# Optimization experiments

Measured on AMD Instinct MI355X. Metric: run time of the kernel, lower is better.

## Reference

```python
import jax, jax.numpy as jnp
import numpy as np

C = 256      # embed_dim
GROUP = 2    # conv groups
K = 3        # kernel/pool size
K2 = K * K
OG = 8       # offset groups (hard-coded in Similarity_cal)
NEX = 3      # exemplars per image (out_conv expects group*3*4 channels)


def conv2d(x, w, b, pad):
    y = jax.lax.conv_general_dilated(x, w, (1, 1), [(pad, pad), (pad, pad)],
                                     dimension_numbers=("NCHW", "OIHW", "NCHW"))
    return y + b[None, :, None, None]


def ln_c(x, g, b, eps=1e-5):
    # LayerNorm over the channel axis of NCHW (torch permutes to NHWC, LN, permute back)
    mu = x.mean(axis=1, keepdims=True)
    var = ((x - mu) ** 2).mean(axis=1, keepdims=True)
    return (x - mu) / jnp.sqrt(var + eps) * g[None, :, None, None] + b[None, :, None, None]


def bilinear_gather(img, py, px):
    # img [Cg,H,W]; py,px [K2,H,W] -> samples [Cg,K2,H,W], zero outside borders
    Cg, H, W = img.shape
    y0f = jnp.floor(py); x0f = jnp.floor(px)
    wy = py - y0f; wx = px - x0f
    y0 = y0f.astype(jnp.int32); x0 = x0f.astype(jnp.int32)
    flat = img.reshape(Cg, H * W)

    def corner(yy, xx, w):
        valid = (yy >= 0) & (yy < H) & (xx >= 0) & (xx < W)
        idx = jnp.clip(yy, 0, H - 1) * W + jnp.clip(xx, 0, W - 1)
        v = jnp.take(flat, idx.reshape(-1), axis=1).reshape(Cg, K2, H, W)
        return v * (w * valid)[None]

    return (corner(y0, x0, (1 - wy) * (1 - wx)) + corner(y0, x0 + 1, (1 - wy) * wx)
            + corner(y0 + 1, x0, wy * (1 - wx)) + corner(y0 + 1, x0 + 1, wy * wx))


def deform_conv(x, offset, mask, weight, dilation):
    # x [C,H,W]; offset [2*OG*K2,H,W]; mask [OG*K2,H,W] (softmaxed); weight [NEX*GROUP, C//GROUP, K, K]
    Cc, H, W = x.shape
    pad = (K - 1) * dilation // 2
    off = offset.reshape(OG, K2, 2, H, W)  # (dy, dx) per offset-group / tap
    kk = jnp.arange(K, dtype=x.dtype)
    ky = jnp.repeat(kk, K) * dilation - pad  # [K2]
    kx = jnp.tile(kk, K) * dilation - pad
    ii = jnp.arange(H, dtype=x.dtype)
    jj = jnp.arange(W, dtype=x.dtype)
    py = ii[None, None, :, None] + ky[None, :, None, None] + off[:, :, 0]  # [OG,K2,H,W]
    px = jj[None, None, None, :] + kx[None, :, None, None] + off[:, :, 1]
    xg = x.reshape(OG, Cc // OG, H, W)
    samp = jax.vmap(bilinear_gather)(xg, py, px)              # [OG,Cg,K2,H,W]
    samp = samp * mask.reshape(OG, 1, K2, H, W)               # modulation
    samp = samp.reshape(GROUP, Cc // GROUP, K2, H, W)
    wR = weight.reshape(NEX * GROUP, Cc // GROUP, K2)
    gidx = jnp.arange(NEX * GROUP) // NEX                     # out-channel -> conv group
    return jnp.einsum("rck,rckhw->rhw", wR, samp[gidx])       # [NEX*GROUP,H,W]


def forward(querys_feat, supports_feat, in_w, in_b, ln_g, ln_b, out_w, out_b,
            offw1, offb1, mskw1, mskb1, offw2, offb2, mskw2, mskb2,
            offw4, offb4, mskw4, mskb4):
    B = querys_feat.shape[0]
    q = ln_c(conv2d(querys_feat, in_w, in_b, 0), ln_g, ln_b)                 # [B,C,H,W]
    s = supports_feat.reshape(B * NEX, C, K, K)
    s = ln_c(conv2d(s, in_w, in_b, 0), ln_g, ln_b).reshape(B, NEX, C, K, K)

    def offs(wo, bo, wm, bm):
        o = conv2d(q, wo, bo, (K - 1) // 2)
        m = jax.nn.softmax(conv2d(q, wm, bm, (K - 1) // 2), axis=1)  # softmax over all OG*K2 channels
        return o, m

    o1, m1 = offs(offw1, offb1, mskw1, mskb1)
    o2, m2 = offs(offw2, offb2, mskw2, mskb2)
    o4, m4 = offs(offw4, offb4, mskw4, mskb4)

    def per_sample(qi, si, o1i, m1i, o2i, m2i, o4i, m4i):
        w = si.reshape(NEX * GROUP, C // GROUP, K, K)         # dynamic per-exemplar kernels
        pooled = si.max(axis=(2, 3)).reshape(NEX * GROUP, C // GROUP)
        gidx = jnp.arange(NEX * GROUP) // NEX
        qg = qi.reshape(GROUP, C // GROUP, *qi.shape[1:])
        sim0 = jnp.einsum("rc,rchw->rhw", pooled, qg[gidx])   # grouped 1x1 conv branch
        d1 = deform_conv(qi, o1i, m1i, w, 1)
        d2 = deform_conv(qi, o2i, m2i, w, 2)
        d4 = deform_conv(qi, o4i, m4i, w, 4)
        return jnp.concatenate([sim0, d1, d2, d4], axis=0)    # [GROUP*3*4, H, W]

    sim = jax.vmap(per_sample)(q, s, o1, m1, o2, m2, o4, m4)
    return conv2d(sim, out_w, out_b, 0)                        # [B,C,H,W]


def setup_inputs() -> dict:
    key = jax.random.key(0)
    ks = jax.random.split(key, 20)
    B, H, W = 2, 96, 96
    inp = {
        "querys_feat": jax.random.normal(ks[0], (B, C, H, W), jnp.float32),
        "supports_feat": jax.random.normal(ks[1], (B, NEX, C, K, K), jnp.float32),
        "in_w": jax.random.normal(ks[2], (C, C, 1, 1), jnp.float32) / 16.0,
        "in_b": jax.random.normal(ks[3], (C,), jnp.float32) * 0.02,
        "ln_g": jnp.ones((C,), jnp.float32),
        "ln_b": jnp.zeros((C,), jnp.float32),
        "out_w": jax.random.normal(ks[4], (C, GROUP * 3 * 4, 1, 1), jnp.float32) * 0.2,
        "out_b": jax.random.normal(ks[5], (C,), jnp.float32) * 0.02,
    }
    i = 6
    for d in (1, 2, 4):
        inp[f"offw{d}"] = jax.random.normal(ks[i], (2 * OG * K2, C, K, K), jnp.float32) * 0.01; i += 1
        inp[f"offb{d}"] = jax.random.normal(ks[i], (2 * OG * K2,), jnp.float32) * 0.1; i += 1
        inp[f"mskw{d}"] = jax.random.normal(ks[i], (OG * K2, C, K, K), jnp.float32) * 0.02; i += 1
        inp[f"mskb{d}"] = jax.random.normal(ks[i], (OG * K2,), jnp.float32) * 0.1; i += 1
    return inp


def reference(querys_feat, supports_feat, in_w, in_b, ln_g, ln_b, out_w, out_b,
              offw1, offb1, mskw1, mskb1, offw2, offb2, mskw2, mskb2,
              offw4, offb4, mskw4, mskb4):
    return forward(querys_feat, supports_feat, in_w, in_b, ln_g, ln_b, out_w, out_b,
                   offw1, offb1, mskw1, mskb1, offw2, offb2, mskw2, mskb2,
                   offw4, offb4, mskw4, mskb4)
```

## Files before the change

### kernel.cpp

```cpp
#include <hip/hip_runtime.h>
#include <hip/hip_bf16.h>
#include <math.h>

#define HH 96
#define WWID 96
#define HW 9216
#define CC 256
#define BB 2
#define PROW 104
#define PCOL 128
#define PPX (PROW * PCOL)

typedef float f32x4 __attribute__((ext_vector_type(4)));
typedef _Float16 f16x8 __attribute__((ext_vector_type(8)));
typedef _Float16 h2v __attribute__((ext_vector_type(2)));

__device__ inline unsigned int pack2h(float a, float b) {
  unsigned short ua = __builtin_bit_cast(unsigned short, (_Float16)a);
  unsigned short ub = __builtin_bit_cast(unsigned short, (_Float16)b);
  return (unsigned int)ua | ((unsigned int)ub << 16);
}
__device__ inline float h_lo(unsigned int u) {
  return (float)__builtin_bit_cast(_Float16, (unsigned short)(u & 0xffffu));
}
__device__ inline float h_hi(unsigned int u) {
  return (float)__builtin_bit_cast(_Float16, (unsigned short)(u >> 16));
}

#if defined(__has_builtin)
#if __has_builtin(__builtin_amdgcn_fdot2)
#define FDOT2(a, b, c) __builtin_amdgcn_fdot2((a), (b), (c), false)
#endif
#endif
#ifndef FDOT2
#define FDOT2(a, b, c) ((c) + (float)(a).x * (float)(b).x + (float)(a).y * (float)(b).y)
#endif

__device__ inline void gload_lds16(const void* g, void* l) {
  __builtin_amdgcn_global_load_lds(
      (const __attribute__((address_space(1))) void*)g,
      (__attribute__((address_space(3))) void*)l, 16, 0, 0);
}

__global__ void k_transpose_w(const float* __restrict__ in_w, float* __restrict__ wT) {
  int k = blockIdx.x, c = threadIdx.x;
  wT[k * CC + c] = in_w[c * CC + k];
}

__global__ void k_packw(const float* __restrict__ ow1, const float* __restrict__ ob1,
                        const float* __restrict__ mw1, const float* __restrict__ mb1,
                        const float* __restrict__ ow2, const float* __restrict__ ob2,
                        const float* __restrict__ mw2, const float* __restrict__ mb2,
                        const float* __restrict__ ow4, const float* __restrict__ ob4,
                        const float* __restrict__ mw4, const float* __restrict__ mb4,
                        _Float16* __restrict__ Whf, float* __restrict__ Ball) {
  int idx = blockIdx.x * 256 + threadIdx.x;
  if (idx >= 3 * 256 * 2304) return;
  int d = idx / (256 * 2304);
  int rem = idx - d * 256 * 2304;
  int co = rem / 2304;
  int k = rem - co * 2304;
  int j = k >> 8, ci = k & 255;
  const float* ow = d == 0 ? ow1 : (d == 1 ? ow2 : ow4);
  const float* mw = d == 0 ? mw1 : (d == 1 ? mw2 : mw4);
  float v = 0.f;
  if (co < 144) v = ow[co * 2304 + ci * 9 + j];
  else if (co < 216) v = mw[(co - 144) * 2304 + ci * 9 + j];
  Whf[idx] = (_Float16)v;
  if (idx < 768) {
    int dd = idx >> 8, cc = idx & 255;
    const float* obv = dd == 0 ? ob1 : (dd == 1 ? ob2 : ob4);
    const float* mbv = dd == 0 ? mb1 : (dd == 1 ? mb2 : mb4);
    float bv = 0.f;
    if (cc < 144) bv = obv[cc];
    else if (cc < 216) bv = mbv[cc - 144];
    Ball[idx] = bv;
  }
}

__global__ void k_conv1_ln_q(const float* __restrict__ qin, const float* __restrict__ wT,
                             const float* __restrict__ in_b, const float* __restrict__ ln_g,
                             const float* __restrict__ ln_b, float* __restrict__ q_hwc,
                             _Float16* __restrict__ qpad) {
  int bx = blockIdx.x;
  int b = bx / 288;
  int hw0 = (bx % 288) * 32;
  int t = threadIdx.x;
  int lane = t & 63;
  int wv_id = t >> 6;
  __shared__ float xs[32 * 260];
  const float* qb = qin + (size_t)b * CC * HW;
  #pragma unroll
  for (int i = 0; i < 32; ++i) {
    int idx = t + i * 256;
    int p = idx & 31;
    int k = idx >> 5;
    xs[p * 260 + k] = qb[k * HW + hw0 + p];
  }
  __syncthreads();
  float acc[8][4];
  #pragma unroll
  for (int p = 0; p < 8; ++p) { acc[p][0]=0.f; acc[p][1]=0.f; acc[p][2]=0.f; acc[p][3]=0.f; }
  const float4* wT4 = (const float4*)wT;
  int p0 = wv_id * 8;
  for (int k = 0; k < 256; k += 4) {
    float4 w0 = wT4[(k + 0) * 64 + lane];
    float4 w1 = wT4[(k + 1) * 64 + lane];
    float4 w2 = wT4[(k + 2) * 64 + lane];
    float4 w3 = wT4[(k + 3) * 64 + lane];
    #pragma unroll
    for (int p = 0; p < 8; ++p) {
      float4 xv = *(const float4*)&xs[(p0 + p) * 260 + k];
      acc[p][0] += w0.x * xv.x + w1.x * xv.y + w2.x * xv.z + w3.x * xv.w;
      acc[p][1] += w0.y * xv.x + w1.y * xv.y + w2.y * xv.z + w3.y * xv.w;
      acc[p][2] += w0.z * xv.x + w1.z * xv.y + w2.z * xv.z + w3.z * xv.w;
      acc[p][3] += w0.w * xv.x + w1.w * xv.y + w2.w * xv.z + w3.w * xv.w;
    }
  }
  float4 bb = ((const float4*)in_b)[lane];
  float4 g4 = ((const float4*)ln_g)[lane];
  float4 b4 = ((const float4*)ln_b)[lane];
  #pragma unroll
  for (int p = 0; p < 8; ++p) {
    float y0 = acc[p][0] + bb.x, y1 = acc[p][1] + bb.y;
    float y2 = acc[p][2] + bb.z, y3 = acc[p][3] + bb.w;
    float s1 = y0 + y1 + y2 + y3;
    float s2 = y0*y0 + y1*y1 + y2*y2 + y3*y3;
    #pragma unroll
    for (int off = 32; off; off >>= 1) { s1 += __shfl_xor(s1, off); s2 += __shfl_xor(s2, off); }
    float mu = s1 * (1.f / 256.f);
    float rstd = rsqrtf(s2 * (1.f / 256.f) - mu * mu + 1e-5f);
    float4 o;
    o.x = (y0 - mu) * rstd * g4.x + b4.x;
    o.y = (y1 - mu) * rstd * g4.y + b4.y;
    o.z = (y2 - mu) * rstd * g4.z + b4.z;
    o.w = (y3 - mu) * rstd * g4.w + b4.w;
    int hw = hw0 + p0 + p;
    ((float4*)q_hwc)[((size_t)b * HW + hw) * 64 + lane] = o;
    int hh = hw / 96, ww = hw - hh * 96;
    int ppx = (hh + 4) * PCOL + ww + 4;
    struct alignas(8) h4 { _Float16 h[4]; };
    h4 oh;
    oh.h[0] = (_Float16)o.x; oh.h[1] = (_Float16)o.y;
    oh.h[2] = (_Float16)o.z; oh.h[3] = (_Float16)o.w;
    *(h4*)(qpad + ((size_t)b * PPX + ppx) * CC + lane * 4) = oh;
  }
}

__global__ void k_conv1_ln_s(const float* __restrict__ sup, const float* __restrict__ wT,
                             const float* __restrict__ in_b, const float* __restrict__ ln_g,
                             const float* __restrict__ ln_b, float* __restrict__ s_ln,
                             float* __restrict__ pooled) {
  int img = blockIdx.x;
  int t = threadIdx.x;
  __shared__ float xs[2304];
  __shared__ float red1[256], red2[256];
  #pragma unroll
  for (int p = 0; p < 9; ++p) xs[t * 9 + p] = sup[(size_t)img * 2304 + t * 9 + p];
  __syncthreads();
  float acc[9];
  #pragma unroll
  for (int p = 0; p < 9; ++p) acc[p] = 0.f;
  for (int k = 0; k < 256; ++k) {
    float wv = wT[k * CC + t];
    #pragma unroll
    for (int p = 0; p < 9; ++p) acc[p] += wv * xs[k * 9 + p];
  }
  float bias = in_b[t];
  #pragma unroll
  for (int p = 0; p < 9; ++p) acc[p] += bias;
  float g = ln_g[t], be = ln_b[t];
  float vals[9];
  #pragma unroll
  for (int p = 0; p < 9; ++p) {
    red1[t] = acc[p]; red2[t] = acc[p] * acc[p];
    __syncthreads();
    for (int s = 128; s > 0; s >>= 1) {
      if (t < s) { red1[t] += red1[t + s]; red2[t] += red2[t + s]; }
      __syncthreads();
    }
    float mu = red1[0] * (1.f / 256.f);
    float var = red2[0] * (1.f / 256.f) - mu * mu;
    float rstd = rsqrtf(var + 1e-5f);
    vals[p] = (acc[p] - mu) * rstd * g + be;
    __syncthreads();
  }
  #pragma unroll
  for (int p = 0; p < 9; ++p) s_ln[(size_t)img * 2304 + t * 9 + p] = vals[p];
  float mx = vals[0];
  #pragma unroll
  for (int p = 1; p < 9; ++p) mx = fmaxf(mx, vals[p]);
  int b = img / 3, e = img % 3;
  pooled[((size_t)b * 6 + e * 2 + (t >> 7)) * 128 + (t & 127)] = mx;
}


#define BAR() __builtin_amdgcn_s_barrier()
#define SCHEDB() __builtin_amdgcn_sched_barrier(0)
#define VMCNT(N) asm volatile("s_waitcnt vmcnt(" #N ")" ::: "memory")

#define MMA_ONE(M, N, S, QM, QN) \
  acc[(QM)*4+(M)][(QN)*2+(N)] = __builtin_amdgcn_mfma_f32_16x16x32_f16( \
      af[M][S], bf[(QN)*2+(N)][S], acc[(QM)*4+(M)][(QN)*2+(N)], 0, 0, 0);

#define MMA_Q(QM, QN) { \
  __builtin_amdgcn_s_setprio(1); \
  MMA_ONE(0,0,0,QM,QN) MMA_ONE(1,0,0,QM,QN) MMA_ONE(2,0,0,QM,QN) MMA_ONE(3,0,0,QM,QN) \
  MMA_ONE(0,1,0,QM,QN) MMA_ONE(1,1,0,QM,QN) MMA_ONE(2,1,0,QM,QN) MMA_ONE(3,1,0,QM,QN) \
  MMA_ONE(0,0,1,QM,QN) MMA_ONE(1,0,1,QM,QN) MMA_ONE(2,0,1,QM,QN) MMA_ONE(3,0,1,QM,QN) \
  MMA_ONE(0,1,1,QM,QN) MMA_ONE(1,1,1,QM,QN) MMA_ONE(2,1,1,QM,QN) MMA_ONE(3,1,1,QM,QN) \
  __builtin_amdgcn_s_setprio(0); }

#define LDA(BUF, QM) { \
  const char* p_ = smemB + (BUF) * 65536 + (wm * 128 + (QM) * 64 + l15) * 128; \
  af[0][0] = *(const f16x8*)(p_ + 0*2048 + rc0); af[0][1] = *(const f16x8*)(p_ + 0*2048 + rc1); \
  af[1][0] = *(const f16x8*)(p_ + 1*2048 + rc0); af[1][1] = *(const f16x8*)(p_ + 1*2048 + rc1); \
  af[2][0] = *(const f16x8*)(p_ + 2*2048 + rc0); af[2][1] = *(const f16x8*)(p_ + 2*2048 + rc1); \
  af[3][0] = *(const f16x8*)(p_ + 3*2048 + rc0); af[3][1] = *(const f16x8*)(p_ + 3*2048 + rc1); }

#define LDB(BUF, QN) { \
  const char* p_ = smemB + (BUF) * 65536 + 32768 + (wn * 64 + (QN) * 32 + l15) * 128; \
  bf[(QN)*2+0][0] = *(const f16x8*)(p_ + 0*2048 + rc0); bf[(QN)*2+0][1] = *(const f16x8*)(p_ + 0*2048 + rc1); \
  bf[(QN)*2+1][0] = *(const f16x8*)(p_ + 1*2048 + rc0); bf[(QN)*2+1][1] = *(const f16x8*)(p_ + 1*2048 + rc1); }

#define STAGEA(TILE, Q) { \
  gload_lds16(aBase + (size_t)((Q) * 64) * 2304 + (TILE) * 64, \
              smemB + ((TILE) & 1) * 65536 + (((Q) * 64 + wv * 8) * 128)); \
  gload_lds16(aBase + (size_t)(128 + (Q) * 64) * 2304 + (TILE) * 64, \
              smemB + ((TILE) & 1) * 65536 + ((128 + (Q) * 64 + wv * 8) * 128)); }

#define STAGEB(TILE, Q, PPX0, PPX1) { \
  int j_ = (TILE) >> 2; \
  int offp_ = (j_ / 3 - 1) * PCOL + (j_ % 3) - 1; \
  int cb_ = ((TILE) & 3) * 64; \
  int rs_ = (wv >> 2) * 64 + (Q) * 32 + (wv & 3) * 8; \
  gload_lds16(bBase + (size_t)((PPX0) + offp_) * CC + cb_, \
              smemB + ((TILE) & 1) * 65536 + 32768 + (rs_ * 128)); \
  gload_lds16(bBase + (size_t)((PPX1) + offp_) * CC + cb_, \
              smemB + ((TILE) & 1) * 65536 + 32768 + ((128 + rs_) * 128)); }

__global__ void __launch_bounds__(512) k_conv3_mfma8(
    const _Float16* __restrict__ qpad, const _Float16* __restrict__ Whf,
    float* __restrict__ offbuf, float* __restrict__ mskbuf) {
  int nb = blockIdx.x;
  int z = blockIdx.y;
  int d = z >> 1, b = z & 1;
  int t = threadIdx.x;
  int lane = t & 63, wv = t >> 6;
  int wm = wv >> 2, wn = wv & 3;
  int quad = lane >> 4, l15 = lane & 15;
  int l8 = lane >> 3, c7 = lane & 7;

  __shared__ _Float16 __attribute__((aligned(16))) smem[65536];
  char* smemB = (char*)smem;

  const _Float16* Wd = Whf + (size_t)d * 256 * 2304;
  const _Float16* qb = qpad + (size_t)b * PPX * CC;

  int scol = ((c7 ^ l8) << 3);
  int rc0 = ((quad ^ (l15 & 7)) << 4);
  int rc1 = (((4 | quad) ^ (l15 & 7)) << 4);

  const _Float16* aBase = Wd + (size_t)(wv * 8 + l8) * 2304 + scol;
  const _Float16* bBase = qb + scol;

  int ppx00, ppx01, ppx10, ppx11;
  {
    int rbase = (wv >> 2) * 64 + (wv & 3) * 8 + l8;
    int px, hh, ww;
    px = nb * 256 + rbase;             hh = px / 96; ww = px - hh * 96; ppx00 = (hh + 4) * PCOL + ww + 4;
    px = nb * 256 + 128 + rbase;       hh = px / 96; ww = px - hh * 96; ppx01 = (hh + 4) * PCOL + ww + 4;
    px = nb * 256 + 32 + rbase;        hh = px / 96; ww = px - hh * 96; ppx10 = (hh + 4) * PCOL + ww + 4;
    px = nb * 256 + 160 + rbase;       hh = px / 96; ww = px - hh * 96; ppx11 = (hh + 4) * PCOL + ww + 4;
  }

  f32x4 acc[8][4];
  #pragma unroll
  for (int i = 0; i < 8; ++i)
    #pragma unroll
    for (int j = 0; j < 4; ++j) acc[i][j] = (f32x4){0.f, 0.f, 0.f, 0.f};

  f16x8 af[4][2], bf[4][2];

  STAGEA(0, 0);
  STAGEB(0, 1, ppx10, ppx11);
  STAGEA(0, 1);
  STAGEB(0, 0, ppx00, ppx01);
  STAGEA(1, 0);
  STAGEB(1, 1, ppx10, ppx11);
  VMCNT(4);
  BAR();
  SCHEDB();

  #pragma unroll 1
  for (int ii = 0; ii < 17; ++ii) {
    int ta = 2 * ii + 1, tb = 2 * ii + 2, tc = 2 * ii + 3;
    LDA(0, 0) LDB(0, 0)
    STAGEA(ta, 1);
    BAR(); MMA_Q(0, 0); BAR();
    LDB(0, 1)
    STAGEB(ta, 0, ppx00, ppx01);
    BAR(); MMA_Q(0, 1); BAR();
    LDA(0, 1)
    STAGEA(tb, 0);
    BAR(); MMA_Q(1, 1); BAR();
    STAGEB(tb, 1, ppx10, ppx11);
    VMCNT(4);
    BAR(); SCHEDB(); MMA_Q(1, 0); BAR();
    LDA(1, 0) LDB(1, 0)
    STAGEA(tb, 1);
    BAR(); MMA_Q(0, 0); BAR();
    LDB(1, 1)
    STAGEB(tb, 0, ppx00, ppx01);
    BAR(); MMA_Q(0, 1); BAR();
    LDA(1, 1)
    STAGEA(tc, 0);
    BAR(); MMA_Q(1, 1); BAR();
    STAGEB(tc, 1, ppx10, ppx11);
    VMCNT(4);
    BAR(); SCHEDB(); MMA_Q(1, 0); BAR();
  }

  LDA(0, 0) LDB(0, 0)
  STAGEA(35, 1);
  BAR(); MMA_Q(0, 0); BAR();
  LDB(0, 1)
  STAGEB(35, 0, ppx00, ppx01);
  BAR(); MMA_Q(0, 1); BAR();
  LDA(0, 1)
  BAR(); MMA_Q(1, 1); BAR();
  VMCNT(0);
  BAR(); SCHEDB(); MMA_Q(1, 0); BAR();
  LDA(1, 0) LDB(1, 0)
  BAR(); MMA_Q(0, 0); BAR();
  LDB(1, 1)
  BAR(); MMA_Q(0, 1); BAR();
  LDA(1, 1)
  BAR(); MMA_Q(1, 1); BAR();
  MMA_Q(1, 0);

  float* obP = offbuf + (size_t)(d * BB + b) * 144 * HW;
  float* mkP = mskbuf + (size_t)(d * BB + b) * 72 * HW;
  #pragma unroll
  for (int mi = 0; mi < 8; ++mi) {
    int co = wm * 128 + mi * 16 + quad * 4;
    #pragma unroll
    for (int ni = 0; ni < 4; ++ni) {
      int px = nb * 256 + wn * 64 + ni * 16 + l15;
      f32x4 v = acc[mi][ni];
      #pragma unroll
      for (int r = 0; r < 4; ++r) {
        int c2 = co + r;
        if (c2 < 144) obP[(size_t)c2 * HW + px] = v[r];
        else if (c2 < 216) mkP[(size_t)(c2 - 144) * HW + px] = v[r];
      }
    }
  }
}

__global__ void k_taps(const float* __restrict__ offbuf, const float* __restrict__ mskbuf,
                       const float* __restrict__ Ball, unsigned int* __restrict__ taprec) {
  int t = threadIdx.x;
  int sub = t & 7, pxl = t >> 3;
  int bx = blockIdx.x;
  int z = bx / 288;
  int px = (bx - z * 288) * 32 + pxl;
  int d = z >> 1;
  const float* Bd = Ball + d * 256;
  const float* mp = mskbuf + (size_t)z * 72 * HW + px;
  float lg[9];
  float mx = -1e30f;
  #pragma unroll
  for (int j = 0; j < 9; ++j) {
    int tk = sub + 8 * j;
    lg[j] = mp[(size_t)tk * HW] + Bd[144 + tk];
    mx = fmaxf(mx, lg[j]);
  }
  mx = fmaxf(mx, __shfl_xor(mx, 1));
  mx = fmaxf(mx, __shfl_xor(mx, 2));
  mx = fmaxf(mx, __shfl_xor(mx, 4));
  float s = 0.f;
  #pragma unroll
  for (int j = 0; j < 9; ++j) s += __expf(lg[j] - mx);
  s += __shfl_xor(s, 1);
  s += __shfl_xor(s, 2);
  s += __shfl_xor(s, 4);
  float rinv = 1.f / s;
  int dil = 1 << (z >> 1);
  int h = px / WWID, w = px - h * WWID;
  const float* ob = offbuf + (size_t)z * 144 * HW + px;
  int k = sub;
  #pragma unroll
  for (int j = 0; j < 9; ++j) {
    int tk = sub + 8 * j;
    float dy = ob[(size_t)(tk * 2 + 0) * HW] + Bd[tk * 2 + 0];
    float dx = ob[(size_t)(tk * 2 + 1) * HW] + Bd[tk * 2 + 1];
    float m = __expf(lg[j] - mx) * rinv;
    float py = (float)(h + (k / 3) * dil - dil) + dy;
    float pxx = (float)(w + (k % 3) * dil - dil) + dx;
    float y0f = floorf(py), x0f = floorf(pxx);
    int y0 = (int)y0f, x0 = (int)x0f;
    float wy = py - y0f, wx = pxx - x0f;
    bool vy0 = (unsigned)y0 < 96u, vy1 = (unsigned)(y0 + 1) < 96u;
    bool vx0 = (unsigned)x0 < 96u, vx1 = (unsigned)(x0 + 1) < 96u;
    float w00 = (vy0 && vx0) ? (1.f - wy) * (1.f - wx) * m : 0.f;
    float w01 = (vy0 && vx1) ? (1.f - wy) * wx * m : 0.f;
    float w10 = (vy1 && vx0) ? wy * (1.f - wx) * m : 0.f;
    float w11 = (vy1 && vx1) ? wy * wx * m : 0.f;
    int iy = min(max(y0 + 4, 0), 102);
    int ix = min(max(x0 + 4, 0), 126);
    unsigned int* r = taprec + (((size_t)(z * 72 + tk)) * HW + px) * 3;
    r[0] = pack2h(w00, w01);
    r[1] = pack2h(w10, w11);
    r[2] = (unsigned int)(iy * PCOL + ix);
    k += 8; if (k >= 9) k -= 9;
  }
}

__global__ void k_sim0(const float* __restrict__ qt, const float* __restrict__ pooled,
                       float* __restrict__ sim) {
  int b = blockIdx.z, h = blockIdx.y, seg = blockIdx.x;
  int t = threadIdx.x;
  int pxl = t >> 5, lane = t & 31;
  int wcol = seg * 8 + pxl;
  int hw = h * WWID + wcol;
  __shared__ float plds[768];
  for (int i = t; i < 768; i += 256) plds[i] = pooled[(size_t)b * 768 + i];
  __syncthreads();
  const float* qtb = qt + (size_t)b * HW * CC;
  float acc[6] = {0.f, 0.f, 0.f, 0.f, 0.f, 0.f};
  #pragma unroll
  for (int m = 0; m < 8; ++m) {
    int cfull = m * 32 + lane;
    float qv = qtb[(size_t)hw * CC + cfull];
    if (m < 4) {
      int cp = cfull;
      acc[0] += plds[0 * 128 + cp] * qv;
      acc[1] += plds[1 * 128 + cp] * qv;
      acc[2] += plds[2 * 128 + cp] * qv;
    } else {
      int cp = cfull - 128;
      acc[3] += plds[3 * 128 + cp] * qv;
      acc[4] += plds[4 * 128 + cp] * qv;
      acc[5] += plds[5 * 128 + cp] * qv;
    }
  }
  #pragma unroll
  for (int r = 0; r < 6; ++r) {
    float v = acc[r];
    #pragma unroll
    for (int off = 16; off; off >>= 1) v += __shfl_down(v, off, 32);
    if (lane == 0) sim[((size_t)b * 24 + r) * HW + hw] = v;
  }
}

#define DO_P(U0, U1, IDX, P) { \
  h2v u0_ = __builtin_bit_cast(h2v, (U0)); \
  h2v u1_ = __builtin_bit_cast(h2v, (U1)); \
  const h2v* b0_ = qc + (size_t)(IDX) * 128; \
  h2v q00_ = b0_[0], q01_ = b0_[128]; \
  h2v q10_ = b0_[16384], q11_ = b0_[16384 + 128]; \
  h2v s_ = q00_ * (h2v){u0_.x, u0_.x} + q01_ * (h2v){u0_.y, u0_.y} \
         + q10_ * (h2v){u1_.x, u1_.x} + q11_ * (h2v){u1_.y, u1_.y}; \
  acc[P][0] = FDOT2(wr0, s_, acc[P][0]); \
  acc[P][1] = FDOT2(wr1, s_, acc[P][1]); \
  acc[P][2] = FDOT2(wr2, s_, acc[P][2]); }

__global__ void __launch_bounds__(256) k_deform(
    const _Float16* __restrict__ qpad, const unsigned int* __restrict__ taprec,
    const float* __restrict__ s_ln, float* __restrict__ sim) {
  int z = blockIdx.z;
  int yhalf = blockIdx.y;
  int d_idx = z >> 1, b = z & 1;
  int seg = blockIdx.x;
  int t = threadIdx.x;
  int g = t >> 5, lane = t & 31;
  int half16 = lane >> 4, l16 = lane & 15;
  __shared__ _Float16 wh[9 * 384];
  int px0 = seg * 32;
  for (int i2 = t; i2 < 3456; i2 += 256) {
    int c = i2 / 9, k = i2 % 9;
    wh[k * 384 + c] = (_Float16)s_ln[(size_t)b * 6912 + yhalf * 3456 + i2];
  }
  __syncthreads();
  int pg = g * 4;
  int pxb = px0 + pg;
  const unsigned int* whd = (const unsigned int*)wh;
  const unsigned int* tz = taprec + (size_t)z * 72 * HW * 3;
  const _Float16* qb = qpad + (size_t)b * PPX * CC;

  float acc[4][3];
  #pragma unroll
  for (int p = 0; p < 4; ++p)
    #pragma unroll
    for (int r = 0; r < 3; ++r) acc[p][r] = 0.f;

  #pragma unroll 1
  for (int ogp = 0; ogp < 2; ++ogp) {
    int og = yhalf * 4 + ogp * 2 + half16;
    int qch = og * 32 + l16 * 2;
    int wcol = qch - yhalf * 128;
    const h2v* qc = (const h2v*)(qb + qch);
    #pragma unroll 3
    for (int k = 0; k < 9; ++k) {
      int tk = og * 9 + k;
      const uint4* rp4 = (const uint4*)(tz + ((size_t)tk * HW + pxb) * 3);
      uint4 ra = rp4[0];
      uint4 rb_ = rp4[1];
      uint4 rc_ = rp4[2];
      h2v wr0 = __builtin_bit_cast(h2v, whd[(k * 384 + 0 + wcol) >> 1]);
      h2v wr1 = __builtin_bit_cast(h2v, whd[(k * 384 + 128 + wcol) >> 1]);
      h2v wr2 = __builtin_bit_cast(h2v, whd[(k * 384 + 256 + wcol) >> 1]);
      DO_P(ra.x, ra.y, ra.z, 0)
      DO_P(ra.w, rb_.x, rb_.y, 1)
      DO_P(rb_.z, rb_.w, rc_.x, 2)
      DO_P(rc_.y, rc_.z, rc_.w, 3)
    }
  }

  #pragma unroll
  for (int p = 0; p < 4; ++p) {
    #pragma unroll
    for (int r = 0; r < 3; ++r) {
      float v = acc[p][r];
      #pragma unroll
      for (int off = 16; off; off >>= 1) v += __shfl_down(v, off, 32);
      if (lane == 0)
        sim[((size_t)b * 24 + 6 + 6 * d_idx + yhalf * 3 + r) * HW + pxb + p] = v;
    }
  }
}

__global__ void k_outconv(const float* __restrict__ sim, const float* __restrict__ out_w,
                          const float* __restrict__ out_b, float* __restrict__ out) {
  int hw = blockIdx.x * 256 + threadIdx.x;
  int co = blockIdx.y, b = blockIdx.z;
  const float* simb = sim + (size_t)b * 24 * HW;
  float a = out_b[co];
  #pragma unroll
  for (int r = 0; r < 24; ++r) a += out_w[co * 24 + r] * simb[(size_t)r * HW + hw];
  out[((size_t)b * CC + co) * HW + hw] = a;
}

extern "C" void kernel_launch(void* const* d_in, const int* in_sizes, int n_in,
                              void* d_out, int out_size, void* d_ws, size_t ws_size,
                              hipStream_t stream) {
  const float* querys = (const float*)d_in[0];
  const float* sup    = (const float*)d_in[1];
  const float* in_w   = (const float*)d_in[2];
  const float* in_b   = (const float*)d_in[3];
  const float* ln_g   = (const float*)d_in[4];
  const float* ln_b   = (const float*)d_in[5];
  const float* out_w  = (const float*)d_in[6];
  const float* out_b  = (const float*)d_in[7];
  const float* ow1 = (const float*)d_in[8];
  const float* ob1 = (const float*)d_in[9];
  const float* mw1 = (const float*)d_in[10];
  const float* mb1 = (const float*)d_in[11];
  const float* ow2 = (const float*)d_in[12];
  const float* ob2 = (const float*)d_in[13];
  const float* mw2 = (const float*)d_in[14];
  const float* mb2 = (const float*)d_in[15];
  const float* ow4 = (const float*)d_in[16];
  const float* ob4 = (const float*)d_in[17];
  const float* mw4 = (const float*)d_in[18];
  const float* mb4 = (const float*)d_in[19];
  float* out = (float*)d_out;

  float* ws_f   = (float*)d_ws;
  float* wT     = ws_f;
  _Float16* Whf = (_Float16*)(wT + 65536);
  float* Ball   = (float*)(Whf + 3 * 256 * 2304);
  float* q_hwc  = Ball + 1024;
  _Float16* qpad = (_Float16*)(q_hwc + (size_t)BB * HW * CC);
  float* s_ln   = (float*)(qpad + (size_t)BB * PPX * CC);
  float* pooled = s_ln + 13824;
  float* offbuf = pooled + 1536;
  float* mskbuf = offbuf + (size_t)3 * BB * 144 * HW;
  float* sim    = mskbuf + (size_t)3 * BB * 72 * HW;
  unsigned int* taprec = (unsigned int*)(sim + (size_t)BB * 24 * HW);

  hipMemsetAsync(qpad, 0, (size_t)BB * PPX * CC * sizeof(_Float16), stream);
  k_transpose_w<<<dim3(256), dim3(256), 0, stream>>>(in_w, wT);
  k_packw<<<dim3((3 * 256 * 2304 + 255) / 256), dim3(256), 0, stream>>>(
      ow1, ob1, mw1, mb1, ow2, ob2, mw2, mb2, ow4, ob4, mw4, mb4, Whf, Ball);
  k_conv1_ln_q<<<dim3(576), dim3(256), 0, stream>>>(querys, wT, in_b, ln_g, ln_b, q_hwc, qpad);
  k_conv1_ln_s<<<dim3(6), dim3(256), 0, stream>>>(sup, wT, in_b, ln_g, ln_b, s_ln, pooled);
  k_conv3_mfma8<<<dim3(36, 6), dim3(512), 0, stream>>>(qpad, Whf, offbuf, mskbuf);
  k_taps<<<dim3(1728), dim3(256), 0, stream>>>(offbuf, mskbuf, Ball, taprec);
  k_sim0<<<dim3(12, 96, BB), dim3(256), 0, stream>>>(q_hwc, pooled, sim);
  k_deform<<<dim3(288, 2, 6), dim3(256), 0, stream>>>(qpad, taprec, s_ln, sim);
  k_outconv<<<dim3(36, 256, BB), dim3(256), 0, stream>>>(sim, out_w, out_b, out);
}
```

Baseline: 383.8 us.

## Stage deform tap records in LDS and remap blocks for XCD locality

The deform kernel now loads each block's 36 taps × 32 pixels of tap records into shared memory with coalesced loads before the main loop. Previously each lane issued strided uint4 global loads per tap. The 3D grid is flattened to 1D, and the block index is decoded so that the low three bits select a slab of segments, which appears aimed at grouping neighbouring pixel segments on the same XCD/L2. The cost is about 13.5KB of extra LDS per block, which may reduce occupancy.

```diff
diff --git a/kernel.cpp b/kernel.cpp
--- a/kernel.cpp
+++ b/kernel.cpp
@@ -469,24 +469,35 @@
 __global__ void __launch_bounds__(256) k_deform(
     const _Float16* __restrict__ qpad, const unsigned int* __restrict__ taprec,
     const float* __restrict__ s_ln, float* __restrict__ sim) {
-  int z = blockIdx.z;
-  int yhalf = blockIdx.y;
+  int bid = blockIdx.x;
+  int slab = bid & 7;
+  int j = bid >> 3;
+  int z = j / 72;
+  int rem = j - z * 72;
+  int yhalf = rem / 36;
+  int segin = rem - yhalf * 36;
+  int seg = slab * 36 + segin;
   int d_idx = z >> 1, b = z & 1;
-  int seg = blockIdx.x;
   int t = threadIdx.x;
   int g = t >> 5, lane = t & 31;
   int half16 = lane >> 4, l16 = lane & 15;
   __shared__ _Float16 wh[9 * 384];
+  __shared__ unsigned int rlds[36 * 96];
   int px0 = seg * 32;
+  int tkbase = yhalf * 36;
+  const unsigned int* tz = taprec + (size_t)z * 72 * HW * 3;
   for (int i2 = t; i2 < 3456; i2 += 256) {
     int c = i2 / 9, k = i2 % 9;
     wh[k * 384 + c] = (_Float16)s_ln[(size_t)b * 6912 + yhalf * 3456 + i2];
+  }
+  for (int i2 = t; i2 < 3456; i2 += 256) {
+    int tko = i2 / 96, dw = i2 - tko * 96;
+    rlds[i2] = tz[((size_t)(tkbase + tko) * HW + px0) * 3 + dw];
   }
   __syncthreads();
   int pg = g * 4;
   int pxb = px0 + pg;
   const unsigned int* whd = (const unsigned int*)wh;
-  const unsigned int* tz = taprec + (size_t)z * 72 * HW * 3;
   const _Float16* qb = qpad + (size_t)b * PPX * CC;
 
   float acc[4][3];
@@ -500,21 +511,18 @@
     int og = yhalf * 4 + ogp * 2 + half16;
     int qch = og * 32 + l16 * 2;
     int wcol = qch - yhalf * 128;
+    int tko = (ogp * 2 + half16) * 9;
     const h2v* qc = (const h2v*)(qb + qch);
     #pragma unroll 3
     for (int k = 0; k < 9; ++k) {
-      int tk = og * 9 + k;
-      const uint4* rp4 = (const uint4*)(tz + ((size_t)tk * HW + pxb) * 3);
-      uint4 ra = rp4[0];
-      uint4 rb_ = rp4[1];
-      uint4 rc_ = rp4[2];
+      const unsigned int* rr = &rlds[(tko + k) * 96 + pg * 3];
       h2v wr0 = __builtin_bit_cast(h2v, whd[(k * 384 + 0 + wcol) >> 1]);
       h2v wr1 = __builtin_bit_cast(h2v, whd[(k * 384 + 128 + wcol) >> 1]);
       h2v wr2 = __builtin_bit_cast(h2v, whd[(k * 384 + 256 + wcol) >> 1]);
-      DO_P(ra.x, ra.y, ra.z, 0)
-      DO_P(ra.w, rb_.x, rb_.y, 1)
-      DO_P(rb_.z, rb_.w, rc_.x, 2)
-      DO_P(rc_.y, rc_.z, rc_.w, 3)
+      DO_P(rr[0], rr[1], rr[2], 0)
+      DO_P(rr[3], rr[4], rr[5], 1)
+      DO_P(rr[6], rr[7], rr[8], 2)
+      DO_P(rr[9], rr[10], rr[11], 3)
     }
   }
 
@@ -589,6 +597,6 @@
   k_conv3_mfma8<<<dim3(36, 6), dim3(512), 0, stream>>>(qpad, Whf, offbuf, mskbuf);
   k_taps<<<dim3(1728), dim3(256), 0, stream>>>(offbuf, mskbuf, Ball, taprec);
   k_sim0<<<dim3(12, 96, BB), dim3(256), 0, stream>>>(q_hwc, pooled, sim);
-  k_deform<<<dim3(288, 2, 6), dim3(256), 0, stream>>>(qpad, taprec, s_ln, sim);
+  k_deform<<<dim3(3456), dim3(256), 0, stream>>>(qpad, taprec, s_ln, sim);
   k_outconv<<<dim3(36, 256, BB), dim3(256), 0, stream>>>(sim, out_w, out_b, out);
 }
```

After: 366.0 us. 1.05x faster.
